# Performance work log

Measured on AMD Instinct MI355X. Metric: run time of the kernel, lower is better.

Reference implementation:

```python
import math
import jax, jax.numpy as jnp
import numpy as np

N_BASIS = 512   # number of basis signals (linear input dim)
FRAME_LEN = 64  # L, basis signal length (linear output dim)
BATCH = 8
FRAMES = 16000


def overlap_and_add(signal, frame_step):
    """Faithful jax port of the torch overlap_and_add (subframe index_add).

    signal: (..., frames, frame_length)
    returns: (..., frame_step*(frames-1)+frame_length)
    """
    *outer, frames, frame_length = signal.shape
    sub_len = math.gcd(frame_length, frame_step)
    sub_step = frame_step // sub_len
    spf = frame_length // sub_len               # subframes per frame
    output_size = frame_step * (frames - 1) + frame_length
    out_sub = output_size // sub_len

    # (..., frames*spf, sub_len)
    subframe_signal = signal.reshape(*outer, frames * spf, sub_len)

    # static scatter indices, same as torch.arange(out_sub).unfold(0, spf, sub_step)
    idx = (np.arange(frames)[:, None] * sub_step + np.arange(spf)[None, :]).reshape(-1)
    idx = jnp.asarray(idx, dtype=jnp.int32)

    result = jnp.zeros((*outer, out_sub, sub_len), dtype=signal.dtype)
    result = result.at[..., idx, :].add(subframe_signal)
    return result.reshape(*outer, out_sub * sub_len)


def setup_inputs() -> dict:
    key = jax.random.key(0)
    k1, k2 = jax.random.split(key)
    weight = jax.random.normal(k1, (BATCH, FRAMES, N_BASIS), dtype=jnp.float32)
    basis_signal_weight = jax.random.normal(k2, (FRAME_LEN, N_BASIS), dtype=jnp.float32)
    return {"weight": weight, "basis_signal_weight": basis_signal_weight}


def reference(weight, basis_signal_weight):
    L = FRAME_LEN
    # nn.Linear with bias=False: source = weight @ W.T ; W: (L, N)
    source = jnp.einsum("bkn,ln->bkl", weight, basis_signal_weight)  # (B, K, L)
    return overlap_and_add(source, L // 2)
```

## Files before the change

kernel.cpp:

```cpp
#include <hip/hip_runtime.h>
#include <hip/hip_bf16.h>

typedef __bf16 bf16x8 __attribute__((ext_vector_type(8)));
typedef __bf16 bf16x4 __attribute__((ext_vector_type(4)));
typedef float  f32x4  __attribute__((ext_vector_type(4)));

#define N_BASIS   512
#define FRAME_LEN 64
#define BATCH     8
#define FRAMES    16000
#define STEP      32
#define OUT_PER_BATCH (STEP * (FRAMES - 1) + FRAME_LEN)

#define WAVES            8
#define BLOCK            (WAVES * 64)
#define FRAMES_PER_BLOCK (WAVES * 16)
#define TILES_PER_BATCH  (FRAMES / FRAMES_PER_BLOCK)

__global__ __launch_bounds__(BLOCK, 4)
void basis_ola_kernel(const float* __restrict__ weight,
                      const float* __restrict__ basis,
                      float* __restrict__ out)
{
    __shared__ __bf16 Wlds[FRAME_LEN * N_BASIS];

    const int tid = threadIdx.x;

    for (int q = tid; q < (FRAME_LEN * N_BASIS) / 4; q += BLOCK) {
        const int e = q * 4;
        const int c = e >> 9;
        const float4 v = *(const float4*)(basis + e);
        bf16x4 b;
        b[0] = (__bf16)v.x; b[1] = (__bf16)v.y;
        b[2] = (__bf16)v.z; b[3] = (__bf16)v.w;
        const int se = e ^ ((c & 7) << 3);
        *(bf16x4*)(&Wlds[se]) = b;
    }
    __syncthreads();

    const int bb   = blockIdx.x / TILES_PER_BATCH;
    const int tile = blockIdx.x % TILES_PER_BATCH;
    const int F0   = tile * FRAMES_PER_BLOCK;

    const int wave = tid >> 6;
    const int lane = tid & 63;
    const int lo   = lane & 15;
    const int hi   = lane >> 4;

    const int frame_row = F0 + wave * 16 + lo;
    const float* arow = weight + ((size_t)bb * FRAMES + frame_row) * (size_t)N_BASIS;

    f32x4 acc[4] = {};

    #pragma unroll 2
    for (int ks = 0; ks < N_BASIS / 32; ++ks) {
        const int kk = ks * 32;

        const float4 a0 = *(const float4*)(arow + kk + hi * 8);
        const float4 a1 = *(const float4*)(arow + kk + hi * 8 + 4);
        bf16x8 af;
        af[0] = (__bf16)a0.x; af[1] = (__bf16)a0.y;
        af[2] = (__bf16)a0.z; af[3] = (__bf16)a0.w;
        af[4] = (__bf16)a1.x; af[5] = (__bf16)a1.y;
        af[6] = (__bf16)a1.z; af[7] = (__bf16)a1.w;

        #pragma unroll
        for (int nt = 0; nt < 4; ++nt) {
            const int c = nt * 16 + lo;
            int e = (c << 9) + kk + hi * 8;
            e ^= (c & 7) << 3;
            const bf16x8 bfr = *(const bf16x8*)(&Wlds[e]);
            acc[nt] = __builtin_amdgcn_mfma_f32_16x16x32_bf16(af, bfr, acc[nt], 0, 0, 0);
        }
    }

    float* ob = out + (size_t)bb * OUT_PER_BATCH;
    const int fbase = F0 + wave * 16 + hi * 4;

    #pragma unroll
    for (int nt = 0; nt < 2; ++nt) {
        atomicAdd(&ob[32 * fbase + nt * 16 + lo], acc[nt][0]);
        #pragma unroll
        for (int r = 1; r < 4; ++r) {
            const int t = 32 * (fbase + r) + nt * 16 + lo;
            ob[t] = acc[nt][r] + acc[nt + 2][r - 1];
        }
        const int t3 = 32 * (fbase + 3) + (nt + 2) * 16 + lo;
        atomicAdd(&ob[t3], acc[nt + 2][3]);
    }
}

extern "C" void kernel_launch(void* const* d_in, const int* in_sizes, int n_in,
                              void* d_out, int out_size, void* d_ws, size_t ws_size,
                              hipStream_t stream) {
    const float* weight = (const float*)d_in[0];
    const float* basis  = (const float*)d_in[1];
    float* out = (float*)d_out;

    hipMemsetAsync(out, 0, (size_t)out_size * sizeof(float), stream);

    const int grid = BATCH * TILES_PER_BATCH;
    basis_ola_kernel<<<grid, BLOCK, 0, stream>>>(weight, basis, out);
}
```

Measured before the change: 61.63 us.

## Replace atomics and memset with in-block halo exchange and recomputed boundary frame

```diff
diff --git a/kernel.cpp b/kernel.cpp
--- a/kernel.cpp
+++ b/kernel.cpp
@@ -14,8 +14,11 @@
 
 #define WAVES            8
 #define BLOCK            (WAVES * 64)
-#define FRAMES_PER_BLOCK (WAVES * 16)
-#define TILES_PER_BATCH  (FRAMES / FRAMES_PER_BLOCK)
+#define FPB              (WAVES * 16)
+#define TPBATCH          (FRAMES / FPB)
+#define TOTAL_TILES      (BATCH * TPBATCH)
+#define TILES_PER_BLOCK  2
+#define GRID             (TOTAL_TILES / TILES_PER_BLOCK)
 
 __global__ __launch_bounds__(BLOCK, 4)
 void basis_ola_kernel(const float* __restrict__ weight,
@@ -23,6 +26,7 @@
                       float* __restrict__ out)
 {
     __shared__ __bf16 Wlds[FRAME_LEN * N_BASIS];
+    __shared__ float xbuf[2][WAVES][2][16];
 
     const int tid = threadIdx.x;
 
@@ -33,60 +37,104 @@
         bf16x4 b;
         b[0] = (__bf16)v.x; b[1] = (__bf16)v.y;
         b[2] = (__bf16)v.z; b[3] = (__bf16)v.w;
-        const int se = e ^ ((c & 7) << 3);
-        *(bf16x4*)(&Wlds[se]) = b;
+        *(bf16x4*)(&Wlds[e ^ ((c & 7) << 3)]) = b;
     }
     __syncthreads();
-
-    const int bb   = blockIdx.x / TILES_PER_BATCH;
-    const int tile = blockIdx.x % TILES_PER_BATCH;
-    const int F0   = tile * FRAMES_PER_BLOCK;
 
     const int wave = tid >> 6;
     const int lane = tid & 63;
     const int lo   = lane & 15;
     const int hi   = lane >> 4;
 
-    const int frame_row = F0 + wave * 16 + lo;
-    const float* arow = weight + ((size_t)bb * FRAMES + frame_row) * (size_t)N_BASIS;
+    const int g0 = blockIdx.x * TILES_PER_BLOCK;
 
-    f32x4 acc[4] = {};
-
-    #pragma unroll 2
-    for (int ks = 0; ks < N_BASIS / 32; ++ks) {
-        const int kk = ks * 32;
-
-        const float4 a0 = *(const float4*)(arow + kk + hi * 8);
-        const float4 a1 = *(const float4*)(arow + kk + hi * 8 + 4);
-        bf16x8 af;
-        af[0] = (__bf16)a0.x; af[1] = (__bf16)a0.y;
-        af[2] = (__bf16)a0.z; af[3] = (__bf16)a0.w;
-        af[4] = (__bf16)a1.x; af[5] = (__bf16)a1.y;
-        af[6] = (__bf16)a1.z; af[7] = (__bf16)a1.w;
-
-        #pragma unroll
-        for (int nt = 0; nt < 4; ++nt) {
-            const int c = nt * 16 + lo;
-            int e = (c << 9) + kk + hi * 8;
-            e ^= (c & 7) << 3;
-            const bf16x8 bfr = *(const bf16x8*)(&Wlds[e]);
-            acc[nt] = __builtin_amdgcn_mfma_f32_16x16x32_bf16(af, bfr, acc[nt], 0, 0, 0);
+    if (wave == 0) {
+        const int bb0 = g0 / TPBATCH, t0 = g0 % TPBATCH;
+        float val = 0.f;
+        if (t0 > 0) {
+            const int c  = 32 + (lane >> 1);
+            const int kh = (lane & 1) * 256;
+            const float* wr = weight + ((size_t)bb0 * FRAMES + (size_t)t0 * FPB - 1) * N_BASIS;
+            for (int n = kh; n < kh + 256; n += 8) {
+                const float4 a0 = *(const float4*)(wr + n);
+                const float4 a1 = *(const float4*)(wr + n + 4);
+                const int e = ((c << 9) + n) ^ ((c & 7) << 3);
+                const bf16x8 bw = *(const bf16x8*)(&Wlds[e]);
+                val += a0.x*(float)bw[0] + a0.y*(float)bw[1] + a0.z*(float)bw[2] + a0.w*(float)bw[3]
+                     + a1.x*(float)bw[4] + a1.y*(float)bw[5] + a1.z*(float)bw[6] + a1.w*(float)bw[7];
+            }
+        }
+        val += __shfl_xor(val, 1);
+        if ((lane & 1) == 0) {
+            const int cc = lane >> 1;
+            xbuf[1][WAVES - 1][cc >> 4][cc & 15] = val;
         }
     }
 
-    float* ob = out + (size_t)bb * OUT_PER_BATCH;
-    const int fbase = F0 + wave * 16 + hi * 4;
+    for (int ti = 0; ti < TILES_PER_BLOCK; ++ti) {
+        const int g    = g0 + ti;
+        const int bb   = g / TPBATCH;
+        const int tile = g % TPBATCH;
+        const int F0   = tile * FPB;
+        const int p    = ti & 1;
 
-    #pragma unroll
-    for (int nt = 0; nt < 2; ++nt) {
-        atomicAdd(&ob[32 * fbase + nt * 16 + lo], acc[nt][0]);
+        const float* arow = weight +
+            ((size_t)bb * FRAMES + F0 + wave * 16 + lo) * (size_t)N_BASIS;
+
+        f32x4 acc[4] = {};
+
+        #pragma unroll 2
+        for (int ks = 0; ks < N_BASIS / 32; ++ks) {
+            const int kk = ks * 32;
+            const float4 a0 = *(const float4*)(arow + kk + hi * 8);
+            const float4 a1 = *(const float4*)(arow + kk + hi * 8 + 4);
+            bf16x8 af;
+            af[0] = (__bf16)a0.x; af[1] = (__bf16)a0.y;
+            af[2] = (__bf16)a0.z; af[3] = (__bf16)a0.w;
+            af[4] = (__bf16)a1.x; af[5] = (__bf16)a1.y;
+            af[6] = (__bf16)a1.z; af[7] = (__bf16)a1.w;
+
+            #pragma unroll
+            for (int nt = 0; nt < 4; ++nt) {
+                const int c = nt * 16 + lo;
+                int e = (c << 9) + kk + hi * 8;
+                e ^= (c & 7) << 3;
+                const bf16x8 bfr = *(const bf16x8*)(&Wlds[e]);
+                acc[nt] = __builtin_amdgcn_mfma_f32_16x16x32_bf16(af, bfr, acc[nt], 0, 0, 0);
+            }
+        }
+
+        if (hi == 3) {
+            xbuf[p][wave][0][lo] = acc[2][3];
+            xbuf[p][wave][1][lo] = acc[3][3];
+        }
+        __syncthreads();
+
+        float* ob = out + (size_t)bb * OUT_PER_BATCH;
+        const int fbase = F0 + wave * 16 + hi * 4;
+
         #pragma unroll
-        for (int r = 1; r < 4; ++r) {
-            const int t = 32 * (fbase + r) + nt * 16 + lo;
-            ob[t] = acc[nt][r] + acc[nt + 2][r - 1];
+        for (int nt = 0; nt < 2; ++nt) {
+            const float up = __shfl_up(acc[nt + 2][3], 16);
+            float pv;
+            if (hi > 0)          pv = up;
+            else if (wave > 0)   pv = xbuf[p][wave - 1][nt][lo];
+            else if (tile > 0)   pv = xbuf[p ^ 1][WAVES - 1][nt][lo];
+            else                 pv = 0.f;
+            ob[32 * fbase + nt * 16 + lo] = acc[nt][0] + pv;
+
+            #pragma unroll
+            for (int r = 1; r < 4; ++r) {
+                ob[32 * (fbase + r) + nt * 16 + lo] = acc[nt][r] + acc[nt + 2][r - 1];
+            }
         }
-        const int t3 = 32 * (fbase + 3) + (nt + 2) * 16 + lo;
-        atomicAdd(&ob[t3], acc[nt + 2][3]);
+
+        if (tile == TPBATCH - 1 && wave == WAVES - 1 && hi == 3) {
+            ob[32 * FRAMES + 0 * 16 + lo] = acc[2][3];
+            ob[32 * FRAMES + 1 * 16 + lo] = acc[3][3];
+        }
+
+        __syncthreads();
     }
 }
 
@@ -97,8 +145,5 @@
     const float* basis  = (const float*)d_in[1];
     float* out = (float*)d_out;
 
-    hipMemsetAsync(out, 0, (size_t)out_size * sizeof(float), stream);
-
-    const int grid = BATCH * TILES_PER_BATCH;
-    basis_ola_kernel<<<grid, BLOCK, 0, stream>>>(weight, basis, out);
+    basis_ola_kernel<<<GRID, BLOCK, 0, stream>>>(weight, basis, out);
 }
```

Measured after the change: 55.30 us. 1.11x faster.
